# Performance work log

Measured on AMD Instinct MI355X. Metric: run time of the kernel, lower is better.

Reference implementation:

```python
import jax, jax.numpy as jnp
import numpy as np

N_NODES = 100000
D = 128


def _sage_layer(h, src, dst, w_self, w_neigh, b):
    # GraphSAGE mean aggregation: mean of neighbor (src) features per dst node.
    msg = h[src]                                            # [E, D] gather
    agg = jax.ops.segment_sum(msg, dst, num_segments=N_NODES)  # [N, D]
    deg = jax.ops.segment_sum(jnp.ones(src.shape, h.dtype), dst, num_segments=N_NODES)
    mean = agg / jnp.maximum(deg, 1.0)[:, None]
    return h @ w_self + mean @ w_neigh + b


def setup_inputs() -> dict:
    key = jax.random.key(0)
    ks = jax.random.split(key, 16)
    E = 1600000
    inp = {
        "feat": jax.random.normal(ks[0], (N_NODES, D), jnp.float32),
        "edge0_src": jax.random.randint(ks[1], (E,), 0, N_NODES),
        "edge0_dst": jax.random.randint(ks[2], (E,), 0, N_NODES),
        "edge1_src": jax.random.randint(ks[3], (E,), 0, N_NODES),
        "edge1_dst": jax.random.randint(ks[4], (E,), 0, N_NODES),
        "pos_src": jax.random.randint(ks[5], (100000,), 0, N_NODES),
        "pos_dst": jax.random.randint(ks[6], (100000,), 0, N_NODES),
        "neg_src": jax.random.randint(ks[7], (500000,), 0, N_NODES),
        "neg_dst": jax.random.randint(ks[8], (500000,), 0, N_NODES),
        # learned parameters
        "w_proj": jax.random.normal(ks[9], (D, D), jnp.float32) / np.sqrt(D),
        "b_proj": jnp.zeros((D,), jnp.float32),
        "w_self1": jax.random.normal(ks[10], (D, D), jnp.float32) / np.sqrt(D),
        "w_neigh1": jax.random.normal(ks[11], (D, D), jnp.float32) / np.sqrt(D),
        "b1": jnp.zeros((D,), jnp.float32),
        "w_self2": jax.random.normal(ks[12], (D, D), jnp.float32) / np.sqrt(D),
        "w_neigh2": jax.random.normal(ks[13], (D, D), jnp.float32) / np.sqrt(D),
        "b2": jnp.zeros((D,), jnp.float32),
    }
    return inp


def reference(feat, edge0_src, edge0_dst, edge1_src, edge1_dst,
              pos_src, pos_dst, neg_src, neg_dst,
              w_proj, b_proj, w_self1, w_neigh1, b1, w_self2, w_neigh2, b2):
    # ProjectionLayer: per-node linear + ReLU on blocks[0].srcdata['feature']
    h = jax.nn.relu(feat @ w_proj + b_proj)
    # GNNLayer: one SAGE-mean layer per block
    h = jax.nn.relu(_sage_layer(h, edge0_src, edge0_dst, w_self1, w_neigh1, b1))
    h = _sage_layer(h, edge1_src, edge1_dst, w_self2, w_neigh2, b2)
    # PredictionLayer: dot-product edge scoring on pos_graph / neg_graph
    pos_score = jnp.sum(h[pos_src] * h[pos_dst], axis=-1)
    neg_score = jnp.sum(h[neg_src] * h[neg_dst], axis=-1)
    return (pos_score, neg_score)
```

## Files before the change

### kernel.cpp

```cpp
#include <hip/hip_runtime.h>
#include <hip/hip_bf16.h>

#define NN 100000
#define DD 128

#define NPB 512
#define NB 196
#define CAPB 12288
#define PA_BLOCKS 196

typedef unsigned short ushort_t;
typedef unsigned int uint_t;
typedef __attribute__((ext_vector_type(8))) short bf16x8;
typedef __attribute__((ext_vector_type(4))) float f32x4;

__device__ __forceinline__ ushort_t f2bf(float f) {
    uint_t u = __builtin_bit_cast(uint_t, f);
    u += 0x7FFFu + ((u >> 16) & 1u);
    return (ushort_t)(u >> 16);
}
__device__ __forceinline__ uint_t pack2bf(float a, float b) {
    return (uint_t)f2bf(a) | ((uint_t)f2bf(b) << 16);
}
__device__ __forceinline__ float bflo(uint_t v) {
    return __builtin_bit_cast(float, v << 16);
}
__device__ __forceinline__ float bfhi(uint_t v) {
    return __builtin_bit_cast(float, v & 0xFFFF0000u);
}

__device__ __forceinline__ void gload16(const ushort_t* g, ushort_t* l) {
    __builtin_amdgcn_global_load_lds(
        (const __attribute__((address_space(1))) void*)g,
        (__attribute__((address_space(3))) void*)l,
        16, 0, 0);
}

#define PREP_W_BLOCKS 320
#define PREP_Z_BLOCKS 3
__global__ __launch_bounds__(256) void prep(
    const float* __restrict__ w_proj,
    const float* __restrict__ w_self1, const float* __restrict__ w_neigh1,
    const float* __restrict__ w_self2, const float* __restrict__ w_neigh2,
    ushort_t* __restrict__ wtp, ushort_t* __restrict__ wt1,
    ushort_t* __restrict__ wt2, int* __restrict__ bcnt,
    ushort_t* __restrict__ h1pad, ushort_t* __restrict__ h2pad)
{
    const int bid = blockIdx.x;
    const int tid = threadIdx.x;
    if (bid < PREP_W_BLOCKS) {
        int which = bid >> 6;
        int t = (bid & 63) * 256 + tid;
        int n = t >> 7, k = t & 127;
        float v;
        ushort_t* d;
        switch (which) {
            case 0: v = w_proj  [(size_t)k * 128 + n]; d = wtp + (size_t)n * 128 + k;       break;
            case 1: v = w_self1 [(size_t)k * 128 + n]; d = wt1 + (size_t)n * 256 + k;       break;
            case 2: v = w_neigh1[(size_t)k * 128 + n]; d = wt1 + (size_t)n * 256 + 128 + k; break;
            case 3: v = w_self2 [(size_t)k * 128 + n]; d = wt2 + (size_t)n * 256 + k;       break;
            default:v = w_neigh2[(size_t)k * 128 + n]; d = wt2 + (size_t)n * 256 + 128 + k; break;
        }
        *d = f2bf(v);
    } else if (bid < PREP_W_BLOCKS + 2) {
        int i = (bid - PREP_W_BLOCKS) * 256 + tid;
        if (i < 2 * NB) bcnt[i] = 0;
    } else {
        uint_t* p1 = (uint_t*)h1pad;
        uint_t* p2 = (uint_t*)h2pad;
        if (tid < 64) p1[tid] = 0;
        else if (tid < 128) p2[tid - 64] = 0;
    }
}

template <bool RELU, bool TWO, bool CVT>
__global__ __launch_bounds__(256, 4) void gemm_bf16(
    const void* __restrict__ Av, const ushort_t* __restrict__ Bm,
    const ushort_t* __restrict__ W, const float* __restrict__ bias,
    ushort_t* __restrict__ outp)
{
    __shared__ char smem[32768];
    ushort_t* At = (ushort_t*)smem;
    ushort_t* Wt = (ushort_t*)(smem + 8192);
    ushort_t* Ot = (ushort_t*)smem;

    const int tid  = threadIdx.x;
    const int lane = tid & 63;
    const int wav  = tid >> 6;
    const int row0 = blockIdx.x * 128;
    const int m0   = (wav & 1) * 64;
    const int n0   = (wav >> 1) * 64;
    const int KTOT = TWO ? 256 : 128;
    const int NCH  = TWO ? 8 : 4;

    f32x4 acc[4][4];
#pragma unroll
    for (int i = 0; i < 4; ++i)
#pragma unroll
        for (int j = 0; j < 4; ++j) acc[i][j] = (f32x4){0.f, 0.f, 0.f, 0.f};

    const int cl = lane & 15;
    const int q  = lane >> 4;

#pragma unroll 1
    for (int ch = 0; ch < NCH; ++ch) {
        const bool second = TWO && (ch >= 4);
        const int kA = (ch & 3) * 32;
        const int kW = ch * 32;

        if (ch) __syncthreads();

        if constexpr (CVT) {
#pragma unroll
            for (int j = 0; j < 2; ++j) {
                int cb = (j * 4 + wav) * 64;
                int c  = cb + lane;
                int r  = c >> 2, k2 = c & 3;
                gload16(W + (size_t)r * KTOT + kW + k2 * 8, Wt + cb * 8);
            }
            uint4 av[2];
            const float* fp = (const float*)Av;
#pragma unroll
            for (int j = 0; j < 2; ++j) {
                int g = tid + 256 * j;
                int r = g >> 2;
                int c = (g & 3) * 8;
                int grow = row0 + r;
                if (grow >= NN) grow = NN - 1;
                float4 f0 = *(const float4*)(fp + (size_t)grow * DD + kA + c);
                float4 f1 = *(const float4*)(fp + (size_t)grow * DD + kA + c + 4);
                av[j].x = pack2bf(f0.x, f0.y);
                av[j].y = pack2bf(f0.z, f0.w);
                av[j].z = pack2bf(f1.x, f1.y);
                av[j].w = pack2bf(f1.z, f1.w);
            }
#pragma unroll
            for (int j = 0; j < 2; ++j) {
                int g = tid + 256 * j;
                int r = g >> 2;
                int c = (g & 3) * 8;
                *(uint4*)(&At[r * 32 + c]) = av[j];
            }
        } else {
            const ushort_t* sp = second ? Bm : (const ushort_t*)Av;
#pragma unroll
            for (int j = 0; j < 2; ++j) {
                int cb = (j * 4 + wav) * 64;
                int c  = cb + lane;
                int r  = c >> 2, k2 = c & 3;
                int grow = row0 + r;
                if (grow >= NN) grow = NN - 1;
                gload16(sp + (size_t)grow * DD + kA + k2 * 8, At + cb * 8);
                gload16(W + (size_t)r * KTOT + kW + k2 * 8, Wt + cb * 8);
            }
        }
        __syncthreads();

        bf16x8 af[4], bfr[4];
#pragma unroll
        for (int i = 0; i < 4; ++i)
            af[i] = *(const bf16x8*)(&At[(m0 + i * 16 + cl) * 32 + q * 8]);
#pragma unroll
        for (int j = 0; j < 4; ++j)
            bfr[j] = *(const bf16x8*)(&Wt[(n0 + j * 16 + cl) * 32 + q * 8]);
#pragma unroll
        for (int i = 0; i < 4; ++i)
#pragma unroll
            for (int j = 0; j < 4; ++j)
                acc[i][j] = __builtin_amdgcn_mfma_f32_16x16x32_bf16(
                    af[i], bfr[j], acc[i][j], 0, 0, 0);
    }

    __syncthreads();
#pragma unroll
    for (int j = 0; j < 4; ++j) {
        int c = n0 + j * 16 + cl;
        float bv = bias[c];
#pragma unroll
        for (int i = 0; i < 4; ++i) {
#pragma unroll
            for (int reg = 0; reg < 4; ++reg) {
                int r = m0 + i * 16 + 4 * q + reg;
                float v = acc[i][j][reg] + bv;
                if constexpr (RELU) v = fmaxf(v, 0.f);
                Ot[r * 128 + c] = f2bf(v);
            }
        }
    }
    __syncthreads();
    int rows = NN - row0; if (rows > 128) rows = 128;
    for (int t = tid; t < rows * 16; t += 256) {
        int r = t >> 4, c8 = (t & 15) * 8;
        *(uint4*)(outp + (size_t)(row0 + r) * DD + c8) =
            *(const uint4*)(&Ot[r * 128 + c8]);
    }
}

__global__ __launch_bounds__(256) void partA2(
    const int* __restrict__ e0s, const int* __restrict__ e0d, int E0,
    const int* __restrict__ e1s, const int* __restrict__ e1d, int E1,
    int* __restrict__ bcnt, uint_t* __restrict__ pairs)
{
    __shared__ int hist[NB];
    __shared__ int base[NB];
    const int tid  = threadIdx.x;
    const int half = blockIdx.x >= PA_BLOCKS;
    const int* __restrict__ src = half ? e1s : e0s;
    const int* __restrict__ dst = half ? e1d : e0d;
    const int E = half ? E1 : E0;
    int* bc = bcnt + half * NB;
    uint_t* pp = pairs + (size_t)half * NB * CAPB;
    const int blk = blockIdx.x - half * PA_BLOCKS;
    const int chunk = (E + PA_BLOCKS - 1) / PA_BLOCKS;
    const int ea = blk * chunk;
    int eb = ea + chunk; if (eb > E) eb = E;

    for (int b = tid; b < NB; b += 256) hist[b] = 0;
    __syncthreads();
    for (int e = ea + tid; e < eb; e += 256)
        atomicAdd(&hist[dst[e] >> 9], 1);
    __syncthreads();
    for (int b = tid; b < NB; b += 256) {
        base[b] = atomicAdd(&bc[b], hist[b]);
        hist[b] = 0;
    }
    __syncthreads();
    for (int e = ea + tid; e < eb; e += 256) {
        int d = dst[e];
        int b = d >> 9;
        int off = atomicAdd(&hist[b], 1);
        int p = base[b] + off;
        if (p < CAPB)
            pp[(size_t)b * CAPB + p] =
                ((uint_t)(d & (NPB - 1)) << 17) | (uint_t)src[e];
    }
}

__global__ __launch_bounds__(256, 2) void partB(
    uint_t* __restrict__ pairs, const int* __restrict__ bcnt,
    int* __restrict__ counts, int* __restrict__ offs)
{
    __shared__ int cnt[NPB];
    __shared__ int loff[NPB];
    __shared__ int ssc[256];
    __shared__ int image[CAPB];

    const int tid  = threadIdx.x;
    const int half = blockIdx.x >= NB;
    const int b    = blockIdx.x - half * NB;
    const int n0   = b << 9;
    int nb = NN - n0; if (nb > NPB) nb = NPB;
    int tot = bcnt[half * NB + b]; if (tot > CAPB) tot = CAPB;
    uint_t* pb = pairs + (size_t)(half * NB + b) * CAPB;
    const int gbase = (half * NB + b) * CAPB;
    int* cnts  = counts + (size_t)half * NN;
    int* offsl = offs   + (size_t)half * NN;

    for (int n = tid; n < NPB; n += 256) cnt[n] = 0;
    __syncthreads();
    for (int i = tid; i < tot; i += 256)
        atomicAdd(&cnt[pb[i] >> 17], 1);
    __syncthreads();

    int a0 = cnt[2 * tid], a1 = cnt[2 * tid + 1];
    int s = a0 + a1;
    ssc[tid] = s;
    __syncthreads();
    for (int off = 1; off < 256; off <<= 1) {
        int t = 0;
        if (tid >= off) t = ssc[tid - off];
        __syncthreads();
        if (tid >= off) ssc[tid] += t;
        __syncthreads();
    }
    int pre = ssc[tid] - s;
    loff[2 * tid]     = pre;
    loff[2 * tid + 1] = pre + a0;
    __syncthreads();

    for (int n = tid; n < nb; n += 256) {
        cnts[n0 + n]  = cnt[n];
        offsl[n0 + n] = gbase + loff[n];
    }
    for (int n = tid; n < NPB; n += 256) cnt[n] = 0;
    __syncthreads();

    for (int i = tid; i < tot; i += 256) {
        uint_t p = pb[i];
        int ln  = p >> 17;
        int pos = loff[ln] + atomicAdd(&cnt[ln], 1);
        image[pos] = (int)(p & 0x1FFFFu);
    }
    __syncthreads();
    for (int i = tid; i < tot; i += 256) pb[i] = (uint_t)image[i];
}

#define AGG_ISSUE(V, J)                                                   \
    do {                                                                  \
        int s_[8];                                                        \
        _Pragma("unroll")                                                 \
        for (int u = 0; u < 8; ++u) {                                     \
            int jj = (J) + u;                                             \
            int jc = jj < cnt ? jj : cnt - 1;                             \
            int sv = (int)csr[start + jc];                                \
            s_[u] = jj < cnt ? sv : NN;                                   \
        }                                                                 \
        _Pragma("unroll")                                                 \
        for (int u = 0; u < 8; ++u)                                       \
            V[u] = *(const uint4*)(hl + (size_t)s_[u] * DD);              \
    } while (0)

#define AGG_ACCUM(V)                                                      \
    do {                                                                  \
        _Pragma("unroll")                                                 \
        for (int u = 0; u < 8; ++u) {                                     \
            a0 += bflo(V[u].x); a1 += bfhi(V[u].x);                       \
            a2 += bflo(V[u].y); a3 += bfhi(V[u].y);                       \
            a4 += bflo(V[u].z); a5 += bfhi(V[u].z);                       \
            a6 += bflo(V[u].w); a7 += bfhi(V[u].w);                       \
        }                                                                 \
    } while (0)

__global__ __launch_bounds__(256) void aggregate_bf16(
    const ushort_t* __restrict__ h, const uint_t* __restrict__ csr,
    const int* __restrict__ offs, const int* __restrict__ counts,
    ushort_t* __restrict__ mean, int nn)
{
    int gid  = blockIdx.x * 256 + threadIdx.x;
    int node = gid >> 4;
    if (node >= nn) return;
    int lane  = gid & 15;
    int start = offs[node];
    int cnt   = counts[node];
    const ushort_t* __restrict__ hl = h + lane * 8;

    float a0 = 0.f, a1 = 0.f, a2 = 0.f, a3 = 0.f;
    float a4 = 0.f, a5 = 0.f, a6 = 0.f, a7 = 0.f;

    int nbt = (cnt + 7) >> 3;
    if (nbt > 0) {
        uint4 va[8], vb[8];
        AGG_ISSUE(va, 0);
        int j = 8, b = 1;
        for (; b + 1 < nbt; b += 2) {
            AGG_ISSUE(vb, j); j += 8;
            AGG_ACCUM(va);
            AGG_ISSUE(va, j); j += 8;
            AGG_ACCUM(vb);
        }
        if (b < nbt) {
            AGG_ISSUE(vb, j);
            AGG_ACCUM(va);
            AGG_ACCUM(vb);
        } else {
            AGG_ACCUM(va);
        }
    }

    float rinv = 1.0f / (float)(cnt > 1 ? cnt : 1);
    uint4 o;
    o.x = pack2bf(a0 * rinv, a1 * rinv);
    o.y = pack2bf(a2 * rinv, a3 * rinv);
    o.z = pack2bf(a4 * rinv, a5 * rinv);
    o.w = pack2bf(a6 * rinv, a7 * rinv);
    *(uint4*)(mean + (size_t)node * DD + lane * 8) = o;
}

__device__ __forceinline__ float dot8(uint4 a, uint4 b) {
    return bflo(a.x) * bflo(b.x) + bfhi(a.x) * bfhi(b.x)
         + bflo(a.y) * bflo(b.y) + bfhi(a.y) * bfhi(b.y)
         + bflo(a.z) * bflo(b.z) + bfhi(a.z) * bfhi(b.z)
         + bflo(a.w) * bflo(b.w) + bfhi(a.w) * bfhi(b.w);
}

__global__ __launch_bounds__(256) void score_both(
    const ushort_t* __restrict__ h,
    const int* __restrict__ ps, const int* __restrict__ pd,
    const int* __restrict__ ns, const int* __restrict__ nd,
    float* __restrict__ out, int EP, int TE)
{
    int gid = blockIdx.x * 256 + threadIdx.x;
    int grp = gid >> 4;
    int e0 = grp * 2;
    if (e0 >= TE) return;
    int lane = gid & 15;
    int e1 = e0 + 1;
    bool has1 = (e1 < TE);
    int ee = has1 ? e1 : e0;

    int s0, d0, s1, d1;
    if (e0 < EP) { s0 = ps[e0]; d0 = pd[e0]; }
    else         { s0 = ns[e0 - EP]; d0 = nd[e0 - EP]; }
    if (ee < EP) { s1 = ps[ee]; d1 = pd[ee]; }
    else         { s1 = ns[ee - EP]; d1 = nd[ee - EP]; }

    const ushort_t* __restrict__ hl = h + lane * 8;
    uint4 va0 = *(const uint4*)(hl + (size_t)s0 * DD);
    uint4 vb0 = *(const uint4*)(hl + (size_t)d0 * DD);
    uint4 va1 = *(const uint4*)(hl + (size_t)s1 * DD);
    uint4 vb1 = *(const uint4*)(hl + (size_t)d1 * DD);

    float r0 = dot8(va0, vb0);
    float r1 = dot8(va1, vb1);
#pragma unroll
    for (int off = 8; off; off >>= 1) {
        r0 += __shfl_down(r0, off, 16);
        r1 += __shfl_down(r1, off, 16);
    }
    if (lane == 0) {
        out[e0] = r0;
        if (has1) out[e1] = r1;
    }
}


extern "C" void kernel_launch(void* const* d_in, const int* in_sizes, int n_in,
                              void* d_out, int out_size, void* d_ws, size_t ws_size,
                              hipStream_t stream)
{
    const float* feat    = (const float*)d_in[0];
    const int*   e0s     = (const int*)d_in[1];
    const int*   e0d     = (const int*)d_in[2];
    const int*   e1s     = (const int*)d_in[3];
    const int*   e1d     = (const int*)d_in[4];
    const int*   ps      = (const int*)d_in[5];
    const int*   pd      = (const int*)d_in[6];
    const int*   ns      = (const int*)d_in[7];
    const int*   nd      = (const int*)d_in[8];
    const float* w_proj  = (const float*)d_in[9];
    const float* b_proj  = (const float*)d_in[10];
    const float* w_self1 = (const float*)d_in[11];
    const float* w_neigh1= (const float*)d_in[12];
    const float* b1      = (const float*)d_in[13];
    const float* w_self2 = (const float*)d_in[14];
    const float* w_neigh2= (const float*)d_in[15];
    const float* b2      = (const float*)d_in[16];

    float* out = (float*)d_out;

    const size_t NF  = (size_t)NN * DD;
    const size_t NFP = NF + DD;
    char* base = (char*)d_ws;

    ushort_t* h3   = (ushort_t*)base;
    ushort_t* h1   = h3 + NFP;
    ushort_t* mean = h1 + NFP;
    ushort_t* h2   = mean + NFP;

    uint_t* pairs  = (uint_t*)(h2 + NFP);
    int*    bcnt   = (int*)(pairs + (size_t)2 * NB * CAPB);
    int*    counts = bcnt + 2 * NB;
    int*    offs   = counts + 2 * NN;
    ushort_t* wts  = (ushort_t*)(offs + 2 * NN);
    ushort_t* wtp = wts;
    ushort_t* wt1 = wts + 128 * 128;
    ushort_t* wt2 = wt1 + 128 * 256;

    const int E0 = in_sizes[1];
    const int E1 = in_sizes[3];
    const int EP = in_sizes[5];
    const int EN = in_sizes[7];

    const int GB  = (NN + 127) / 128;
    const int AGB = (NN * 16 + 255) / 256;

    prep<<<PREP_W_BLOCKS + PREP_Z_BLOCKS, 256, 0, stream>>>(
        w_proj, w_self1, w_neigh1, w_self2, w_neigh2, wtp, wt1, wt2, bcnt,
        h1 + NF, h2 + NF);

    partA2<<<2 * PA_BLOCKS, 256, 0, stream>>>(
        e0s, e0d, E0, e1s, e1d, E1, bcnt, pairs);
    partB<<<2 * NB, 256, 0, stream>>>(pairs, bcnt, counts, offs);

    gemm_bf16<true, false, true><<<GB, 256, 0, stream>>>(
        feat, nullptr, wtp, b_proj, h1);

    aggregate_bf16<<<AGB, 256, 0, stream>>>(h1, pairs, offs, counts, mean, NN);
    gemm_bf16<true, true, false><<<GB, 256, 0, stream>>>(
        h1, mean, wt1, b1, h2);

    aggregate_bf16<<<AGB, 256, 0, stream>>>(
        h2, pairs, offs + NN, counts + NN, mean, NN);
    gemm_bf16<false, true, false><<<GB, 256, 0, stream>>>(
        h2, mean, wt2, b2, h3);

    const int TE = EP + EN;
    const int NG = (TE + 1) / 2;
    score_both<<<(NG * 16 + 255) / 256, 256, 0, stream>>>(
        h3, ps, pd, ns, nd, out, EP, TE);
}
```

Before: 402.6 us.

## Process multiple nodes per aggregation thread group with cross-node load pipelining

Each 16-lane group in the mean aggregation now handles several nodes (strided by the slot count) rather than one. The double-buffered gather keeps issuing the next 8-neighbor batch across node boundaries, so loads for the next node overlap accumulation of the current one, and it finalizes each node's mean when its last batch is accumulated. This is meant to hide gather latency at node tails and cut per-node startup cost, at the price of fewer threads and more control flow. It relies on NN being divisible by the per-thread node count.

```diff
diff --git a/kernel.cpp b/kernel.cpp
--- a/kernel.cpp
+++ b/kernel.cpp
@@ -295,13 +295,15 @@
     for (int i = tid; i < tot; i += 256) pb[i] = (uint_t)image[i];
 }
 
-#define AGG_ISSUE(V, J)                                                   \
+#define AGG_NPT 5
+
+#define AGG_ISSUE(V)                                                      \
     do {                                                                  \
         int s_[8];                                                        \
         _Pragma("unroll")                                                 \
         for (int u = 0; u < 8; ++u) {                                     \
-            int jj = (J) + u;                                             \
-            int jc = jj < cnt ? jj : cnt - 1;                             \
+            int jj = j + u;                                               \
+            int jc = jj < cnt ? jj : 0;                                   \
             int sv = (int)csr[start + jc];                                \
             s_[u] = jj < cnt ? sv : NN;                                   \
         }                                                                 \
@@ -321,49 +323,81 @@
         }                                                                 \
     } while (0)
 
+#define AGG_ADV()                                                         \
+    do {                                                                  \
+        j += 8;                                                           \
+        if (j >= cnt) {                                                   \
+            ++k; j = 0;                                                   \
+            if (k < AGG_NPT) {                                            \
+                node  = slot + k * nslot;                                 \
+                start = offs[node];                                       \
+                cnt   = counts[node];                                     \
+            }                                                             \
+        }                                                                 \
+    } while (0)
+
+#define AGG_FIN(CNT, NODE)                                                \
+    do {                                                                  \
+        float rinv = 1.0f / (float)((CNT) > 1 ? (CNT) : 1);               \
+        uint4 o;                                                          \
+        o.x = pack2bf(a0 * rinv, a1 * rinv);                              \
+        o.y = pack2bf(a2 * rinv, a3 * rinv);                              \
+        o.z = pack2bf(a4 * rinv, a5 * rinv);                              \
+        o.w = pack2bf(a6 * rinv, a7 * rinv);                              \
+        *(uint4*)(mean + (size_t)(NODE) * DD + lane * 8) = o;             \
+        a0 = a1 = a2 = a3 = a4 = a5 = a6 = a7 = 0.f;                      \
+    } while (0)
+
 __global__ __launch_bounds__(256) void aggregate_bf16(
     const ushort_t* __restrict__ h, const uint_t* __restrict__ csr,
     const int* __restrict__ offs, const int* __restrict__ counts,
-    ushort_t* __restrict__ mean, int nn)
+    ushort_t* __restrict__ mean, int nslot)
 {
     int gid  = blockIdx.x * 256 + threadIdx.x;
-    int node = gid >> 4;
-    if (node >= nn) return;
-    int lane  = gid & 15;
+    int slot = gid >> 4;
+    if (slot >= nslot) return;
+    int lane = gid & 15;
+    const ushort_t* __restrict__ hl = h + lane * 8;
+
+    float a0 = 0.f, a1 = 0.f, a2 = 0.f, a3 = 0.f;
+    float a4 = 0.f, a5 = 0.f, a6 = 0.f, a7 = 0.f;
+
+    uint4 va[8], vb[8];
+
+    int k     = 0;
+    int node  = slot;
     int start = offs[node];
     int cnt   = counts[node];
-    const ushort_t* __restrict__ hl = h + lane * 8;
-
-    float a0 = 0.f, a1 = 0.f, a2 = 0.f, a3 = 0.f;
-    float a4 = 0.f, a5 = 0.f, a6 = 0.f, a7 = 0.f;
-
-    int nbt = (cnt + 7) >> 3;
-    if (nbt > 0) {
-        uint4 va[8], vb[8];
-        AGG_ISSUE(va, 0);
-        int j = 8, b = 1;
-        for (; b + 1 < nbt; b += 2) {
-            AGG_ISSUE(vb, j); j += 8;
+    int j     = 0;
+
+    AGG_ISSUE(va);
+    bool lastA = (j + 8 >= cnt); int cntA = cnt; int nodeA = node;
+    bool lastB = false;          int cntB = 0;   int nodeB = 0;
+    AGG_ADV();
+
+    bool par = false;
+    while (true) {
+        bool more = (k < AGG_NPT);
+        if (!par) {
+            if (more) {
+                AGG_ISSUE(vb);
+                lastB = (j + 8 >= cnt); cntB = cnt; nodeB = node;
+                AGG_ADV();
+            }
             AGG_ACCUM(va);
-            AGG_ISSUE(va, j); j += 8;
+            if (lastA) AGG_FIN(cntA, nodeA);
+        } else {
+            if (more) {
+                AGG_ISSUE(va);
+                lastA = (j + 8 >= cnt); cntA = cnt; nodeA = node;
+                AGG_ADV();
+            }
             AGG_ACCUM(vb);
+            if (lastB) AGG_FIN(cntB, nodeB);
         }
-        if (b < nbt) {
-            AGG_ISSUE(vb, j);
-            AGG_ACCUM(va);
-            AGG_ACCUM(vb);
-        } else {
-            AGG_ACCUM(va);
-        }
-    }
-
-    float rinv = 1.0f / (float)(cnt > 1 ? cnt : 1);
-    uint4 o;
-    o.x = pack2bf(a0 * rinv, a1 * rinv);
-    o.y = pack2bf(a2 * rinv, a3 * rinv);
-    o.z = pack2bf(a4 * rinv, a5 * rinv);
-    o.w = pack2bf(a6 * rinv, a7 * rinv);
-    *(uint4*)(mean + (size_t)node * DD + lane * 8) = o;
+        if (!more) break;
+        par = !par;
+    }
 }
 
 __device__ __forceinline__ float dot8(uint4 a, uint4 b) {
@@ -461,8 +495,9 @@
     const int EP = in_sizes[5];
     const int EN = in_sizes[7];
 
-    const int GB  = (NN + 127) / 128;
-    const int AGB = (NN * 16 + 255) / 256;
+    const int GB    = (NN + 127) / 128;
+    const int NSLOT = NN / AGG_NPT;
+    const int AGB   = (NSLOT * 16 + 255) / 256;
 
     prep<<<PREP_W_BLOCKS + PREP_Z_BLOCKS, 256, 0, stream>>>(
         w_proj, w_self1, w_neigh1, w_self2, w_neigh2, wtp, wt1, wt2, bcnt,
@@ -475,12 +510,12 @@
     gemm_bf16<true, false, true><<<GB, 256, 0, stream>>>(
         feat, nullptr, wtp, b_proj, h1);
 
-    aggregate_bf16<<<AGB, 256, 0, stream>>>(h1, pairs, offs, counts, mean, NN);
+    aggregate_bf16<<<AGB, 256, 0, stream>>>(h1, pairs, offs, counts, mean, NSLOT);
     gemm_bf16<true, true, false><<<GB, 256, 0, stream>>>(
         h1, mean, wt1, b1, h2);
 
     aggregate_bf16<<<AGB, 256, 0, stream>>>(
-        h2, pairs, offs + NN, counts + NN, mean, NN);
+        h2, pairs, offs + NN, counts + NN, mean, NSLOT);
     gemm_bf16<false, true, false><<<GB, 256, 0, stream>>>(
         h2, mean, wt2, b2, h3);
 
```

New measurement: 431.8 us. +7.2%, slower.

## Double-buffer LDS tiles in non-converting bf16 GEMM to overlap loads with MFMA

Applied to the files above, without the earlier changes.

For the non-CVT GEMM variants, the single LDS staging buffer becomes two 16KB buffers. The next K-chunk is issued with direct global-to-LDS loads while the current chunk runs through the MFMA loop, with one wait and barrier per iteration instead of two syncs. This aims to hide global load latency behind compute, but the GEMMs are a small part of a gather/scatter-dominated pipeline, and LDS use per block stays at 32KB.

```diff
diff --git a/kernel.cpp b/kernel.cpp
--- a/kernel.cpp
+++ b/kernel.cpp
@@ -80,8 +80,6 @@
     ushort_t* __restrict__ outp)
 {
     __shared__ char smem[32768];
-    ushort_t* At = (ushort_t*)smem;
-    ushort_t* Wt = (ushort_t*)(smem + 8192);
     ushort_t* Ot = (ushort_t*)smem;
 
     const int tid  = threadIdx.x;
@@ -102,15 +100,15 @@
     const int cl = lane & 15;
     const int q  = lane >> 4;
 
+    if constexpr (CVT) {
+        ushort_t* At = (ushort_t*)smem;
+        ushort_t* Wt = (ushort_t*)(smem + 8192);
 #pragma unroll 1
-    for (int ch = 0; ch < NCH; ++ch) {
-        const bool second = TWO && (ch >= 4);
-        const int kA = (ch & 3) * 32;
-        const int kW = ch * 32;
-
-        if (ch) __syncthreads();
-
-        if constexpr (CVT) {
+        for (int ch = 0; ch < NCH; ++ch) {
+            const int kA = (ch & 3) * 32;
+            const int kW = ch * 32;
+
+            if (ch) __syncthreads();
 #pragma unroll
             for (int j = 0; j < 2; ++j) {
                 int cb = (j * 4 + wav) * 64;
@@ -141,7 +139,29 @@
                 int c = (g & 3) * 8;
                 *(uint4*)(&At[r * 32 + c]) = av[j];
             }
-        } else {
+            __syncthreads();
+
+            bf16x8 af[4], bfr[4];
+#pragma unroll
+            for (int i = 0; i < 4; ++i)
+                af[i] = *(const bf16x8*)(&At[(m0 + i * 16 + cl) * 32 + q * 8]);
+#pragma unroll
+            for (int j = 0; j < 4; ++j)
+                bfr[j] = *(const bf16x8*)(&Wt[(n0 + j * 16 + cl) * 32 + q * 8]);
+#pragma unroll
+            for (int i = 0; i < 4; ++i)
+#pragma unroll
+                for (int j = 0; j < 4; ++j)
+                    acc[i][j] = __builtin_amdgcn_mfma_f32_16x16x32_bf16(
+                        af[i], bfr[j], acc[i][j], 0, 0, 0);
+        }
+    } else {
+        auto STAGE = [&](int ch, int buf) {
+            const bool second = TWO && (ch >= 4);
+            const int kA = (ch & 3) * 32;
+            const int kW = ch * 32;
+            ushort_t* At = (ushort_t*)(smem + buf * 16384);
+            ushort_t* Wt = At + 4096;
             const ushort_t* sp = second ? Bm : (const ushort_t*)Av;
 #pragma unroll
             for (int j = 0; j < 2; ++j) {
@@ -153,22 +173,38 @@
                 gload16(sp + (size_t)grow * DD + kA + k2 * 8, At + cb * 8);
                 gload16(W + (size_t)r * KTOT + kW + k2 * 8, Wt + cb * 8);
             }
+        };
+        auto COMPUTE = [&](int buf) {
+            ushort_t* At = (ushort_t*)(smem + buf * 16384);
+            ushort_t* Wt = At + 4096;
+            bf16x8 af[4], bfr[4];
+#pragma unroll
+            for (int i = 0; i < 4; ++i)
+                af[i] = *(const bf16x8*)(&At[(m0 + i * 16 + cl) * 32 + q * 8]);
+#pragma unroll
+            for (int j = 0; j < 4; ++j)
+                bfr[j] = *(const bf16x8*)(&Wt[(n0 + j * 16 + cl) * 32 + q * 8]);
+#pragma unroll
+            for (int i = 0; i < 4; ++i)
+#pragma unroll
+                for (int j = 0; j < 4; ++j)
+                    acc[i][j] = __builtin_amdgcn_mfma_f32_16x16x32_bf16(
+                        af[i], bfr[j], acc[i][j], 0, 0, 0);
+        };
+
+        STAGE(0, 0);
+        asm volatile("s_waitcnt vmcnt(0)" ::: "memory");
+        __builtin_amdgcn_s_barrier();
+        int cur = 0;
+#pragma unroll 1
+        for (int ch = 0; ch < NCH - 1; ++ch) {
+            STAGE(ch + 1, cur ^ 1);
+            COMPUTE(cur);
+            asm volatile("s_waitcnt vmcnt(0)" ::: "memory");
+            __builtin_amdgcn_s_barrier();
+            cur ^= 1;
         }
-        __syncthreads();
-
-        bf16x8 af[4], bfr[4];
-#pragma unroll
-        for (int i = 0; i < 4; ++i)
-            af[i] = *(const bf16x8*)(&At[(m0 + i * 16 + cl) * 32 + q * 8]);
-#pragma unroll
-        for (int j = 0; j < 4; ++j)
-            bfr[j] = *(const bf16x8*)(&Wt[(n0 + j * 16 + cl) * 32 + q * 8]);
-#pragma unroll
-        for (int i = 0; i < 4; ++i)
-#pragma unroll
-            for (int j = 0; j < 4; ++j)
-                acc[i][j] = __builtin_amdgcn_mfma_f32_16x16x32_bf16(
-                    af[i], bfr[j], acc[i][j], 0, 0, 0);
+        COMPUTE(cur);
     }
 
     __syncthreads();
```

New measurement: 398.8 us. About the same (-0.9%).
